# Kernel optimization log

Measured on AMD Instinct MI355X. Metric: run time of the kernel, lower is better.

## Reference

```python
import jax, jax.numpy as jnp
import numpy as np

BETA = 0.25
N_E = 8192
E_DIM = 64
B, L = 32, 512


def setup_inputs() -> dict:
    key = jax.random.key(0)
    k1, k2, k3 = jax.random.split(key, 3)
    z = jax.random.normal(k1, (B, E_DIM, L), dtype=jnp.float32)
    mask = jax.random.randint(k2, (B, L), 0, 2, dtype=jnp.int32)
    # nn.Embedding init: uniform(-1/n_e, 1/n_e)
    emb = jax.random.uniform(k3, (N_E, E_DIM), dtype=jnp.float32,
                             minval=-1.0 / N_E, maxval=1.0 / N_E)
    return {"z": z, "mask": mask, "emb": emb}


def reference(z, mask, emb):
    sg = jax.lax.stop_gradient
    b, c, l = z.shape            # c == e_dim
    n_e = emb.shape[0]
    zt = jnp.transpose(z, (0, 2, 1))          # (B, L, C)
    zf = zt.reshape(-1, c)                    # (B*L, C)
    m = mask.reshape(-1, 1).astype(zf.dtype)  # (B*L, 1) per-token mask

    # pairwise squared distances (with masked z, as in original)
    zm = zf * m
    d = (jnp.sum(zf * zf * m, axis=1, keepdims=True)
         + jnp.sum(emb * emb, axis=1)
         - 2.0 * jnp.matmul(zm, emb.T))       # (B*L, n_e)

    idx = jnp.argmin(d, axis=1)               # (B*L,)
    min_encodings = jax.nn.one_hot(idx, n_e, dtype=zf.dtype)  # (B*L, n_e)
    z_q = emb[idx].reshape(zt.shape)          # gather == one_hot @ emb

    # masked MSE losses (mask broadcast over the C dim, mean over mask.sum()*C)
    m3 = m.reshape(b, l, 1)
    denom = jnp.sum(m3) * c
    embedding_loss = jnp.sum((sg(z_q) - zt) ** 2 * m3) / denom
    commitment_loss = jnp.sum((z_q - sg(zt)) ** 2 * m3) / denom
    loss = embedding_loss + BETA * commitment_loss

    # straight-through estimator
    z_q_st = zt + sg(z_q - zt)

    e_mean = jnp.mean(min_encodings, axis=0)
    perplexity = jnp.exp(-jnp.sum(e_mean * jnp.log(e_mean + 1e-10)))

    z_q_out = jnp.transpose(z_q_st, (0, 2, 1))  # back to (B, C, L)
    return loss, z_q_out, perplexity, min_encodings, idx[:, None]
```

## Files before the change

kernel.cpp:

```cpp
#include <hip/hip_runtime.h>
#include <cstdint>
#include <cstddef>

#define TOK 16384
#define NE  8192

#define O_ZQ   1
#define O_PERP 1048577
#define O_ENC  1048578
#define O_IDX  135266306

__global__ __launch_bounds__(256) void k_init(
    const float* __restrict__ z, const int* __restrict__ mask,
    const float* __restrict__ emb,
    unsigned long long* __restrict__ packed,
    float* __restrict__ s_z, float* __restrict__ s_e,
    int* __restrict__ hist) {
  int g = blockIdx.x * 256 + threadIdx.x;
  if (g < TOK) {
    int t = g, b = t >> 9, l = t & 511;
    const float* zp = z + (size_t)b * 32768 + l;
    float r[8];
#pragma unroll
    for (int j = 0; j < 8; ++j) { float v = zp[(size_t)j * 512]; r[j] = __fmul_rn(v, v); }
#pragma unroll
    for (int i = 8; i < 64; i += 8)
#pragma unroll
      for (int j = 0; j < 8; ++j) { float v = zp[(size_t)(i + j) * 512]; r[j] = __fadd_rn(r[j], __fmul_rn(v, v)); }
    float s = __fadd_rn(__fadd_rn(__fadd_rn(r[0], r[1]), __fadd_rn(r[2], r[3])),
                        __fadd_rn(__fadd_rn(r[4], r[5]), __fadd_rn(r[6], r[7])));
    s_z[t] = mask[t] ? s : 0.0f;
    packed[t] = ~0ull;
  } else if (g < TOK + NE) {
    int i = g - TOK;
    const float* ep = emb + (size_t)i * 64;
    float r[8];
#pragma unroll
    for (int j = 0; j < 8; ++j) { float v = ep[j]; r[j] = __fmul_rn(v, v); }
#pragma unroll
    for (int kk = 8; kk < 64; kk += 8)
#pragma unroll
      for (int j = 0; j < 8; ++j) { float v = ep[kk + j]; r[j] = __fadd_rn(r[j], __fmul_rn(v, v)); }
    float s = __fadd_rn(__fadd_rn(__fadd_rn(r[0], r[1]), __fadd_rn(r[2], r[3])),
                        __fadd_rn(__fadd_rn(r[4], r[5]), __fadd_rn(r[6], r[7])));
    s_e[i] = s;
    hist[i] = 0;
  }
}

__global__ __launch_bounds__(256, 2) void k_search(
    const float* __restrict__ z, const int* __restrict__ mask,
    const float* __restrict__ emb,
    const float* __restrict__ s_z, const float* __restrict__ s_e,
    unsigned long long* __restrict__ packed,
    float* __restrict__ enc_out) {
  __shared__ __align__(16) float zs[128][68];
  __shared__ __align__(16) float es[128][68];

  const int tid = threadIdx.x;
  const int I0  = blockIdx.x * 128;
  const int T0  = blockIdx.y * 128;
  const int b   = T0 >> 9;
  const int l0  = T0 & 511;

  {
    float* encb = enc_out + (size_t)T0 * 8192 + I0;
#pragma unroll
    for (int it = 0; it < 16; ++it) {
      int id  = it * 256 + tid;
      int row = id >> 5;
      int c4  = id & 31;
      *(float4*)(encb + (size_t)row * 8192 + c4 * 4) = make_float4(0.f, 0.f, 0.f, 0.f);
    }
  }

  {
    const int lq = tid & 127;
    const int m  = mask[T0 + lq];
#pragma unroll
    for (int rep = 0; rep < 32; ++rep) {
      int c = (tid >> 7) + rep * 2;
      float v = z[(size_t)b * 32768 + (size_t)c * 512 + l0 + lq];
      zs[lq][c] = m ? v : 0.0f;
    }
  }
  {
    const int cq = tid & 63;
#pragma unroll
    for (int rep = 0; rep < 32; ++rep) {
      int i = (tid >> 6) + rep * 4;
      es[i][cq] = emb[(size_t)(I0 + i) * 64 + cq];
    }
  }
  __syncthreads();

  const int tg = tid >> 4;
  const int cg = tid & 15;

  float acc[8][8];
#pragma unroll
  for (int m = 0; m < 8; ++m)
#pragma unroll
    for (int j = 0; j < 8; ++j) acc[m][j] = 0.0f;

#pragma unroll 1
  for (int kc = 0; kc < 64; kc += 4) {
    float4 zv[8];
#pragma unroll
    for (int m = 0; m < 8; ++m) zv[m] = *(const float4*)&zs[tg + 16 * m][kc];

#pragma unroll
    for (int jj = 0; jj < 2; ++jj) {
      float4 ev[4];
#pragma unroll
      for (int q = 0; q < 4; ++q) ev[q] = *(const float4*)&es[cg + 16 * (jj * 4 + q)][kc];
#pragma unroll
      for (int m = 0; m < 8; ++m)
#pragma unroll
        for (int q = 0; q < 4; ++q) {
          const int j = jj * 4 + q;
          acc[m][j] = fmaf(zv[m].x, ev[q].x, acc[m][j]);
          acc[m][j] = fmaf(zv[m].y, ev[q].y, acc[m][j]);
          acc[m][j] = fmaf(zv[m].z, ev[q].z, acc[m][j]);
          acc[m][j] = fmaf(zv[m].w, ev[q].w, acc[m][j]);
        }
    }
  }

  float szv[8], sev[8];
#pragma unroll
  for (int m = 0; m < 8; ++m) szv[m] = s_z[T0 + tg + 16 * m];
#pragma unroll
  for (int j = 0; j < 8; ++j) sev[j] = s_e[I0 + cg + 16 * j];

  float best_d[8];
  int   best_i[8];
#pragma unroll
  for (int m = 0; m < 8; ++m) { best_d[m] = __uint_as_float(0x7F800000u); best_i[m] = 0; }
#pragma unroll
  for (int j = 0; j < 8; ++j) {
    const int i = I0 + cg + 16 * j;
#pragma unroll
    for (int m = 0; m < 8; ++m) {
      float d = __fsub_rn(__fadd_rn(szv[m], sev[j]), __fmul_rn(2.0f, acc[m][j]));
      bool lt = d < best_d[m];
      best_d[m] = lt ? d : best_d[m];
      best_i[m] = lt ? i : best_i[m];
    }
  }

#pragma unroll
  for (int m = 0; m < 8; ++m) {
    unsigned int db = __float_as_uint(best_d[m]);
    db = ((int)db < 0) ? ~db : (db | 0x80000000u);
    unsigned long long p = ((unsigned long long)db << 32) | (unsigned int)best_i[m];
#pragma unroll
    for (int off = 1; off < 16; off <<= 1) {
      unsigned long long q = __shfl_xor(p, off, 64);
      p = (q < p) ? q : p;
    }
    if (cg == 0) atomicMin(&packed[T0 + tg + 16 * m], p);
  }
}

__global__ __launch_bounds__(512) void k_finalize(
    const float* __restrict__ z, const int* __restrict__ mask,
    const float* __restrict__ emb,
    const unsigned long long* __restrict__ packed,
    float* __restrict__ out_zq, float* __restrict__ out_enc,
    float* __restrict__ out_idx,
    int* __restrict__ hist, float* __restrict__ token_loss) {
  __shared__ float part[8][64];
  const int T0   = blockIdx.x * 64;
  const int lane = threadIdx.x & 63;
  const int w    = threadIdx.x >> 6;
  const int b    = T0 >> 9;
  const int l0   = T0 & 511;
  const int t    = T0 + lane;

  const int idx = (int)(unsigned int)(packed[t] & 0xFFFFFFFFu);

  const float* zb = z      + (size_t)b * 32768 + l0 + lane;
  float*       qb = out_zq + (size_t)b * 32768 + l0 + lane;

  float sq = 0.0f;
#pragma unroll
  for (int cc = 0; cc < 8; ++cc) {
    int c = w * 8 + cc;
    float zv   = zb[(size_t)c * 512];
    float e    = emb[(size_t)idx * 64 + c];
    float diff = __fsub_rn(e, zv);
    qb[(size_t)c * 512] = __fadd_rn(zv, diff);
    sq = fmaf(diff, diff, sq);
  }
  part[w][lane] = sq;
  __syncthreads();

  if (w == 0) {
    float s = __fadd_rn(
        __fadd_rn(__fadd_rn(part[0][lane], part[1][lane]),
                  __fadd_rn(part[2][lane], part[3][lane])),
        __fadd_rn(__fadd_rn(part[4][lane], part[5][lane]),
                  __fadd_rn(part[6][lane], part[7][lane])));
    token_loss[t] = mask[t] ? s : 0.0f;
    out_idx[t] = (float)idx;
    out_enc[(size_t)t * 8192 + idx] = 1.0f;
    atomicAdd(&hist[idx], 1);
  }
}

__global__ __launch_bounds__(256) void k_partial(
    const float* __restrict__ token_loss, const int* __restrict__ mask,
    const int* __restrict__ hist, float* __restrict__ partials) {
  __shared__ float sf[256], sm[256], sh[256];
  const int bb = blockIdx.x, tid = threadIdx.x;
  int ti = bb * 256 + tid;
  sf[tid] = token_loss[ti];
  sm[tid] = (float)mask[ti];
  float h = 0.f;
  if (tid < 128) {
    float pm = (float)hist[bb * 128 + tid] * (1.0f / 16384.0f);
    h = pm * logf(pm + 1e-10f);
  }
  sh[tid] = h;
  __syncthreads();
  for (int off = 128; off; off >>= 1) {
    if (tid < off) { sf[tid] += sf[tid + off]; sm[tid] += sm[tid + off]; sh[tid] += sh[tid + off]; }
    __syncthreads();
  }
  if (tid == 0) {
    partials[bb]       = sf[0];
    partials[64 + bb]  = sm[0];
    partials[128 + bb] = sh[0];
  }
}

__global__ __launch_bounds__(64) void k_final(
    const float* __restrict__ partials, float* __restrict__ out) {
  int tn = threadIdx.x;
  float lo = partials[tn], mc = partials[64 + tn], en = partials[128 + tn];
#pragma unroll
  for (int off = 32; off; off >>= 1) {
    lo += __shfl_down(lo, off, 64);
    mc += __shfl_down(mc, off, 64);
    en += __shfl_down(en, off, 64);
  }
  if (tn == 0) {
    float denom = mc * 64.0f;
    float el = lo / denom;
    out[0]      = __fadd_rn(el, __fmul_rn(0.25f, el));
    out[O_PERP] = expf(-en);
  }
}

extern "C" void kernel_launch(void* const* d_in, const int* in_sizes, int n_in,
                              void* d_out, int out_size, void* d_ws, size_t ws_size,
                              hipStream_t stream) {
  const float* z    = (const float*)d_in[0];
  const int*   mask = (const int*)d_in[1];
  const float* emb  = (const float*)d_in[2];
  float* out = (float*)d_out;
  char*  ws  = (char*)d_ws;

  unsigned long long* packed = (unsigned long long*)ws;
  float* s_z        = (float*)(ws + 131072);
  float* s_e        = (float*)(ws + 196608);
  int*   hist       = (int*)  (ws + 229376);
  float* token_loss = (float*)(ws + 262144);
  float* partials   = (float*)(ws + 327680);

  k_init<<<96, 256, 0, stream>>>(z, mask, emb, packed, s_z, s_e, hist);

  dim3 g1(64, 128, 1);
  k_search<<<g1, 256, 0, stream>>>(z, mask, emb, s_z, s_e, packed, out + O_ENC);

  k_finalize<<<256, 512, 0, stream>>>(z, mask, emb, packed,
                                      out + O_ZQ, out + O_ENC, out + O_IDX,
                                      hist, token_loss);

  k_partial<<<64, 256, 0, stream>>>(token_loss, mask, hist, partials);
  k_final<<<1, 64, 0, stream>>>(partials, out);
}
```

Before: 363.7 us.

## Use bf16 MFMA coarse search with per-tile minima then exact fp32 refinement

Replaces the fp32 FMA distance GEMM with a bf16 MFMA pass that records only per-token, per-256-code-tile minimum distances. A window kernel sets a per-token threshold from those minima. An exact fp32 kernel then recomputes distances only for tiles whose coarse minimum falls within that threshold. Masked tokens take a shortcut: their index is the code with the smallest norm, found once in init. This aims to cut the heavy fp32 GEMM cost, but relies on the fixed 1e-3 window covering the bf16 error, and the refinement cost depends on the data.

```diff
diff --git a/kernel.cpp b/kernel.cpp
--- a/kernel.cpp
+++ b/kernel.cpp
@@ -4,18 +4,33 @@
 
 #define TOK 16384
 #define NE  8192
+#define NTILE 32
+#define WWIN 1e-3f
 
 #define O_ZQ   1
 #define O_PERP 1048577
 #define O_ENC  1048578
 #define O_IDX  135266306
+
+typedef short bf16x8 __attribute__((ext_vector_type(8)));
+typedef float f32x4  __attribute__((ext_vector_type(4)));
+
+__device__ __forceinline__ unsigned short f2bf(float v) {
+  unsigned int u = __float_as_uint(v);
+  return (unsigned short)((u + 0x7FFFu + ((u >> 16) & 1u)) >> 16);
+}
+
+__global__ void k_zero(unsigned long long* se_min) {
+  if (threadIdx.x == 0) *se_min = ~0ull;
+}
 
 __global__ __launch_bounds__(256) void k_init(
     const float* __restrict__ z, const int* __restrict__ mask,
     const float* __restrict__ emb,
     unsigned long long* __restrict__ packed,
     float* __restrict__ s_z, float* __restrict__ s_e,
-    int* __restrict__ hist) {
+    int* __restrict__ hist, unsigned int* __restrict__ tilemin,
+    unsigned long long* __restrict__ se_min) {
   int g = blockIdx.x * 256 + threadIdx.x;
   if (g < TOK) {
     int t = g, b = t >> 9, l = t & 511;
@@ -31,6 +46,10 @@
                         __fadd_rn(__fadd_rn(r[4], r[5]), __fadd_rn(r[6], r[7])));
     s_z[t] = mask[t] ? s : 0.0f;
     packed[t] = ~0ull;
+    uint4 inf4 = make_uint4(0x7F800000u, 0x7F800000u, 0x7F800000u, 0x7F800000u);
+    uint4* tmi = (uint4*)(tilemin + (size_t)t * NTILE);
+#pragma unroll
+    for (int i = 0; i < 8; ++i) tmi[i] = inf4;
   } else if (g < TOK + NE) {
     int i = g - TOK;
     const float* ep = emb + (size_t)i * 64;
@@ -45,121 +64,214 @@
                         __fadd_rn(__fadd_rn(r[4], r[5]), __fadd_rn(r[6], r[7])));
     s_e[i] = s;
     hist[i] = 0;
-  }
-}
-
-__global__ __launch_bounds__(256, 2) void k_search(
+    unsigned long long p = ((unsigned long long)__float_as_uint(s) << 32) | (unsigned int)i;
+    atomicMin(se_min, p);
+  }
+}
+
+__global__ __launch_bounds__(256, 2) void k_mfma(
     const float* __restrict__ z, const int* __restrict__ mask,
     const float* __restrict__ emb,
     const float* __restrict__ s_z, const float* __restrict__ s_e,
-    unsigned long long* __restrict__ packed,
-    float* __restrict__ enc_out) {
-  __shared__ __align__(16) float zs[128][68];
-  __shared__ __align__(16) float es[128][68];
+    unsigned int* __restrict__ tilemin, float* __restrict__ enc_out) {
+  __shared__ __align__(16) unsigned short zs[128][64];
+  __shared__ __align__(16) unsigned short es[64][64];
 
   const int tid = threadIdx.x;
-  const int I0  = blockIdx.x * 128;
+  const int I0  = blockIdx.x * 64;
   const int T0  = blockIdx.y * 128;
   const int b   = T0 >> 9;
   const int l0  = T0 & 511;
 
   {
-    float* encb = enc_out + (size_t)T0 * 8192 + I0;
-#pragma unroll
-    for (int it = 0; it < 16; ++it) {
-      int id  = it * 256 + tid;
-      int row = id >> 5;
-      int c4  = id & 31;
+    const int tok = tid & 127, kh = tid >> 7;
+    const int mt  = mask[T0 + tok];
+    const float* zp = z + (size_t)b * 32768 + l0 + tok;
+#pragma unroll
+    for (int i = 0; i < 4; ++i) {
+      int k0 = kh * 32 + i * 8;
+      unsigned int w0 = 0, w1 = 0, w2 = 0, w3 = 0;
+      {
+        float v0 = mt ? zp[(size_t)(k0 + 0) * 512] : 0.0f;
+        float v1 = mt ? zp[(size_t)(k0 + 1) * 512] : 0.0f;
+        float v2 = mt ? zp[(size_t)(k0 + 2) * 512] : 0.0f;
+        float v3 = mt ? zp[(size_t)(k0 + 3) * 512] : 0.0f;
+        float v4 = mt ? zp[(size_t)(k0 + 4) * 512] : 0.0f;
+        float v5 = mt ? zp[(size_t)(k0 + 5) * 512] : 0.0f;
+        float v6 = mt ? zp[(size_t)(k0 + 6) * 512] : 0.0f;
+        float v7 = mt ? zp[(size_t)(k0 + 7) * 512] : 0.0f;
+        w0 = (unsigned int)f2bf(v0) | ((unsigned int)f2bf(v1) << 16);
+        w1 = (unsigned int)f2bf(v2) | ((unsigned int)f2bf(v3) << 16);
+        w2 = (unsigned int)f2bf(v4) | ((unsigned int)f2bf(v5) << 16);
+        w3 = (unsigned int)f2bf(v6) | ((unsigned int)f2bf(v7) << 16);
+      }
+      int slot = (k0 >> 3) ^ (tok & 7);
+      *(uint4*)&zs[tok][slot * 8] = make_uint4(w0, w1, w2, w3);
+    }
+  }
+  {
+    const int code = tid >> 2, q = tid & 3;
+    const float* ep = emb + (size_t)(I0 + code) * 64 + q * 16;
+    unsigned int w[8];
+#pragma unroll
+    for (int j = 0; j < 8; ++j)
+      w[j] = (unsigned int)f2bf(ep[2 * j]) | ((unsigned int)f2bf(ep[2 * j + 1]) << 16);
+    int s0 = (q * 2) ^ (code & 7), s1 = (q * 2 + 1) ^ (code & 7);
+    *(uint4*)&es[code][s0 * 8] = make_uint4(w[0], w[1], w[2], w[3]);
+    *(uint4*)&es[code][s1 * 8] = make_uint4(w[4], w[5], w[6], w[7]);
+  }
+  __syncthreads();
+
+  const int l  = tid & 63, w = tid >> 6;
+  const int wr = w >> 1, wc = w & 1;
+  const int rA = l & 15;
+  const int kg = l >> 4;
+
+  f32x4 acc[4][2];
+#pragma unroll
+  for (int fr = 0; fr < 4; ++fr)
+#pragma unroll
+    for (int fc = 0; fc < 2; ++fc)
+#pragma unroll
+      for (int r = 0; r < 4; ++r) acc[fr][fc][r] = 0.0f;
+
+  float* encb = enc_out + (size_t)T0 * 8192 + I0;
+
+#pragma unroll
+  for (int q = 0; q < 2; ++q) {
+    bf16x8 af[4], bfv[2];
+#pragma unroll
+    for (int fr = 0; fr < 4; ++fr) {
+      int row  = wr * 64 + fr * 16 + rA;
+      int slot = (q * 4 + kg) ^ (row & 7);
+      af[fr] = *(const bf16x8*)&zs[row][slot * 8];
+    }
+#pragma unroll
+    for (int fc = 0; fc < 2; ++fc) {
+      int crow = wc * 32 + fc * 16 + rA;
+      int slot = (q * 4 + kg) ^ (crow & 7);
+      bfv[fc] = *(const bf16x8*)&es[crow][slot * 8];
+    }
+#pragma unroll
+    for (int fr = 0; fr < 4; ++fr)
+#pragma unroll
+      for (int fc = 0; fc < 2; ++fc)
+        acc[fr][fc] = __builtin_amdgcn_mfma_f32_16x16x32_bf16(af[fr], bfv[fc], acc[fr][fc], 0, 0, 0);
+
+#pragma unroll
+    for (int it = 0; it < 4; ++it) {
+      int id  = (q * 4 + it) * 256 + tid;
+      int row = id >> 4, c4 = id & 15;
       *(float4*)(encb + (size_t)row * 8192 + c4 * 4) = make_float4(0.f, 0.f, 0.f, 0.f);
     }
   }
 
-  {
-    const int lq = tid & 127;
-    const int m  = mask[T0 + lq];
-#pragma unroll
-    for (int rep = 0; rep < 32; ++rep) {
-      int c = (tid >> 7) + rep * 2;
-      float v = z[(size_t)b * 32768 + (size_t)c * 512 + l0 + lq];
-      zs[lq][c] = m ? v : 0.0f;
-    }
-  }
-  {
-    const int cq = tid & 63;
-#pragma unroll
-    for (int rep = 0; rep < 32; ++rep) {
-      int i = (tid >> 6) + rep * 4;
-      es[i][cq] = emb[(size_t)(I0 + i) * 64 + cq];
-    }
+  float se2[2];
+#pragma unroll
+  for (int fc = 0; fc < 2; ++fc) se2[fc] = s_e[I0 + wc * 32 + fc * 16 + rA];
+  const int tslot = blockIdx.x >> 2;
+
+#pragma unroll
+  for (int fr = 0; fr < 4; ++fr) {
+#pragma unroll
+    for (int r = 0; r < 4; ++r) {
+      int tok = T0 + wr * 64 + fr * 16 + kg * 4 + r;
+      float szv = s_z[tok];
+      float d0 = (szv + se2[0]) - 2.0f * acc[fr][0][r];
+      float d1 = (szv + se2[1]) - 2.0f * acc[fr][1][r];
+      float dm = fminf(d0, d1);
+      dm = fminf(dm, __shfl_xor(dm, 1, 64));
+      dm = fminf(dm, __shfl_xor(dm, 2, 64));
+      dm = fminf(dm, __shfl_xor(dm, 4, 64));
+      dm = fminf(dm, __shfl_xor(dm, 8, 64));
+      if (rA == 0)
+        atomicMin(&tilemin[(size_t)tok * NTILE + tslot], __float_as_uint(dm));
+    }
+  }
+}
+
+__global__ __launch_bounds__(256) void k_window(
+    const int* __restrict__ mask, const unsigned int* __restrict__ tilemin,
+    const unsigned long long* __restrict__ se_min,
+    unsigned long long* __restrict__ packed, float* __restrict__ thresh) {
+  int t = blockIdx.x * 256 + threadIdx.x;
+  if (mask[t]) {
+    unsigned int mn = 0xFFFFFFFFu;
+    const uint4* tm = (const uint4*)(tilemin + (size_t)t * NTILE);
+#pragma unroll
+    for (int i = 0; i < 8; ++i) {
+      uint4 v = tm[i];
+      mn = min(mn, min(min(v.x, v.y), min(v.z, v.w)));
+    }
+    thresh[t] = __uint_as_float(mn) + WWIN;
+  } else {
+    packed[t] = *se_min;
+    thresh[t] = -1.0f;
+  }
+}
+
+__global__ __launch_bounds__(256) void k_exact(
+    const float* __restrict__ z, const float* __restrict__ emb,
+    const float* __restrict__ s_z, const float* __restrict__ s_e,
+    const unsigned int* __restrict__ tilemin, const float* __restrict__ thresh,
+    unsigned long long* __restrict__ packed) {
+  __shared__ float el[256][65];
+  const int tile = blockIdx.x;
+  const int C0   = tile * 256;
+  const int tid  = threadIdx.x, l = tid & 63, w = tid >> 6;
+
+#pragma unroll
+  for (int it = 0; it < 16; ++it) {
+    int idx = it * 256 + tid;
+    int code = idx >> 4, kq = idx & 15;
+    float4 v = *(const float4*)(emb + (size_t)(C0 + code) * 64 + kq * 4);
+    el[code][kq * 4 + 0] = v.x;
+    el[code][kq * 4 + 1] = v.y;
+    el[code][kq * 4 + 2] = v.z;
+    el[code][kq * 4 + 3] = v.w;
   }
   __syncthreads();
 
-  const int tg = tid >> 4;
-  const int cg = tid & 15;
-
-  float acc[8][8];
-#pragma unroll
-  for (int m = 0; m < 8; ++m)
-#pragma unroll
-    for (int j = 0; j < 8; ++j) acc[m][j] = 0.0f;
-
-#pragma unroll 1
-  for (int kc = 0; kc < 64; kc += 4) {
-    float4 zv[8];
-#pragma unroll
-    for (int m = 0; m < 8; ++m) zv[m] = *(const float4*)&zs[tg + 16 * m][kc];
-
-#pragma unroll
-    for (int jj = 0; jj < 2; ++jj) {
-      float4 ev[4];
-#pragma unroll
-      for (int q = 0; q < 4; ++q) ev[q] = *(const float4*)&es[cg + 16 * (jj * 4 + q)][kc];
-#pragma unroll
-      for (int m = 0; m < 8; ++m)
-#pragma unroll
-        for (int q = 0; q < 4; ++q) {
-          const int j = jj * 4 + q;
-          acc[m][j] = fmaf(zv[m].x, ev[q].x, acc[m][j]);
-          acc[m][j] = fmaf(zv[m].y, ev[q].y, acc[m][j]);
-          acc[m][j] = fmaf(zv[m].z, ev[q].z, acc[m][j]);
-          acc[m][j] = fmaf(zv[m].w, ev[q].w, acc[m][j]);
-        }
-    }
-  }
-
-  float szv[8], sev[8];
-#pragma unroll
-  for (int m = 0; m < 8; ++m) szv[m] = s_z[T0 + tg + 16 * m];
-#pragma unroll
-  for (int j = 0; j < 8; ++j) sev[j] = s_e[I0 + cg + 16 * j];
-
-  float best_d[8];
-  int   best_i[8];
-#pragma unroll
-  for (int m = 0; m < 8; ++m) { best_d[m] = __uint_as_float(0x7F800000u); best_i[m] = 0; }
-#pragma unroll
-  for (int j = 0; j < 8; ++j) {
-    const int i = I0 + cg + 16 * j;
-#pragma unroll
-    for (int m = 0; m < 8; ++m) {
-      float d = __fsub_rn(__fadd_rn(szv[m], sev[j]), __fmul_rn(2.0f, acc[m][j]));
-      bool lt = d < best_d[m];
-      best_d[m] = lt ? d : best_d[m];
-      best_i[m] = lt ? i : best_i[m];
-    }
-  }
-
-#pragma unroll
-  for (int m = 0; m < 8; ++m) {
-    unsigned int db = __float_as_uint(best_d[m]);
-    db = ((int)db < 0) ? ~db : (db | 0x80000000u);
-    unsigned long long p = ((unsigned long long)db << 32) | (unsigned int)best_i[m];
-#pragma unroll
-    for (int off = 1; off < 16; off <<= 1) {
-      unsigned long long q = __shfl_xor(p, off, 64);
-      p = (q < p) ? q : p;
-    }
-    if (cg == 0) atomicMin(&packed[T0 + tg + 16 * m], p);
+  const int gw   = blockIdx.y * 4 + w;
+  const int base = gw * 512;
+
+  for (int s = 0; s < 8; ++s) {
+    int tt = base + s * 64 + l;
+    float th = thresh[tt];
+    float tf = __uint_as_float(tilemin[(size_t)tt * NTILE + tile]);
+    unsigned long long bal = __ballot(tf <= th);
+    while (bal) {
+      int bit = __ffsll((long long)bal) - 1;
+      bal &= bal - 1;
+      int t = base + s * 64 + bit;
+      float zreg = z[(size_t)(t >> 9) * 32768 + (size_t)l * 512 + (t & 511)];
+      float szt  = s_z[t];
+      float a0 = 0.f, a1 = 0.f, a2 = 0.f, a3 = 0.f;
+      for (int k = 0; k < 64; ++k) {
+        float zk = __shfl(zreg, k, 64);
+        a0 = fmaf(el[l][k], zk, a0);
+        a1 = fmaf(el[l + 64][k], zk, a1);
+        a2 = fmaf(el[l + 128][k], zk, a2);
+        a3 = fmaf(el[l + 192][k], zk, a3);
+      }
+      unsigned long long best = ~0ull;
+      float av[4] = {a0, a1, a2, a3};
+#pragma unroll
+      for (int c = 0; c < 4; ++c) {
+        int code = C0 + l + 64 * c;
+        float d = __fsub_rn(__fadd_rn(szt, s_e[code]), __fmul_rn(2.0f, av[c]));
+        unsigned int db = __float_as_uint(d);
+        db = ((int)db < 0) ? ~db : (db | 0x80000000u);
+        unsigned long long p = ((unsigned long long)db << 32) | (unsigned int)code;
+        best = (p < best) ? p : best;
+      }
+#pragma unroll
+      for (int off = 1; off < 64; off <<= 1) {
+        unsigned long long q = __shfl_xor(best, off, 64);
+        best = (q < best) ? q : best;
+      }
+      if (l == 0) atomicMin(&packed[t], best);
+    }
   }
 }
 
@@ -262,17 +374,26 @@
   float* out = (float*)d_out;
   char*  ws  = (char*)d_ws;
 
-  unsigned long long* packed = (unsigned long long*)ws;
-  float* s_z        = (float*)(ws + 131072);
-  float* s_e        = (float*)(ws + 196608);
-  int*   hist       = (int*)  (ws + 229376);
-  float* token_loss = (float*)(ws + 262144);
-  float* partials   = (float*)(ws + 327680);
-
-  k_init<<<96, 256, 0, stream>>>(z, mask, emb, packed, s_z, s_e, hist);
-
-  dim3 g1(64, 128, 1);
-  k_search<<<g1, 256, 0, stream>>>(z, mask, emb, s_z, s_e, packed, out + O_ENC);
+  unsigned long long* packed  = (unsigned long long*)ws;
+  float*              s_z     = (float*)(ws + 131072);
+  float*              s_e     = (float*)(ws + 196608);
+  int*                hist    = (int*)(ws + 229376);
+  float*              token_loss = (float*)(ws + 262144);
+  float*              partials   = (float*)(ws + 327680);
+  unsigned long long* se_min  = (unsigned long long*)(ws + 331776);
+  float*              thresh  = (float*)(ws + 335872);
+  unsigned int*       tilemin = (unsigned int*)(ws + 401408);
+
+  k_zero<<<1, 64, 0, stream>>>(se_min);
+  k_init<<<96, 256, 0, stream>>>(z, mask, emb, packed, s_z, s_e, hist, tilemin, se_min);
+
+  dim3 gm(128, 128, 1);
+  k_mfma<<<gm, 256, 0, stream>>>(z, mask, emb, s_z, s_e, tilemin, out + O_ENC);
+
+  k_window<<<64, 256, 0, stream>>>(mask, tilemin, se_min, packed, thresh);
+
+  dim3 ge(32, 8, 1);
+  k_exact<<<ge, 256, 0, stream>>>(z, emb, s_z, s_e, tilemin, thresh, packed);
 
   k_finalize<<<256, 512, 0, stream>>>(z, mask, emb, packed,
                                       out + O_ZQ, out + O_ENC, out + O_IDX,
```

After: 792.7 us. 2.18x slower.
